# Performance work log

Hardware: AMD Instinct MI355X
Metric: run time of the kernel (lower is better)

Reference implementation:

```python
import jax, jax.numpy as jnp
import numpy as np

B, N, K, D, H = 16384, 10, 5, 512, 2
HD = D // H  # 256
IMG = 512.0


def setup_inputs() -> dict:
    key = jax.random.key(0)
    ks = jax.random.split(key, 18)
    w = lambda k, shape: (jax.random.normal(k, shape) * 0.02).astype(jnp.float32)
    boxes = jax.random.uniform(ks[0], (B, N, 4), minval=0.0, maxval=IMG, dtype=jnp.float32)
    return {
        'boxes': boxes,
        'w_in': w(ks[1], (D, K * 4)), 'b_in': jnp.zeros((D,), jnp.float32),
        'wqkv': w(ks[2], (3 * D, D)), 'bqkv': jnp.zeros((3 * D,), jnp.float32),
        'wo': w(ks[3], (D, D)), 'bo': jnp.zeros((D,), jnp.float32),
        'ln1_w': jnp.ones((D,), jnp.float32), 'ln1_b': jnp.zeros((D,), jnp.float32),
        'w1': w(ks[4], (D, D)), 'b1': jnp.zeros((D,), jnp.float32),
        'w2': w(ks[5], (D, D)), 'b2': jnp.zeros((D,), jnp.float32),
        'ln2_w': jnp.ones((D,), jnp.float32), 'ln2_b': jnp.zeros((D,), jnp.float32),
        'lnf_w': jnp.ones((D,), jnp.float32), 'lnf_b': jnp.zeros((D,), jnp.float32),
    }


def _ln(x, w, b, eps=1e-5):
    mu = jnp.mean(x, -1, keepdims=True)
    var = jnp.mean((x - mu) ** 2, -1, keepdims=True)
    return (x - mu) * jax.lax.rsqrt(var + eps) * w + b


def _relationships(boxes):
    # boxes: [B, N, 4] -> rel: [B, N, K*4]
    cx = (boxes[..., 0] + boxes[..., 2]) * 0.5 / IMG
    cy = (boxes[..., 1] + boxes[..., 3]) * 0.5 / IMG
    bw = jnp.abs(boxes[..., 2] - boxes[..., 0]) / IMG
    bh = jnp.abs(boxes[..., 3] - boxes[..., 1]) / IMG
    feats = jnp.stack([cx, cy, bw, bh], -1)  # [B, N, 4]
    dx = cx[:, :, None] - cx[:, None, :]
    dy = cy[:, :, None] - cy[:, None, :]
    dists = dx * dx + dy * dy  # [B, N, N]
    dists = jnp.where(jnp.eye(N, dtype=bool), jnp.inf, dists)
    _, idx = jax.lax.top_k(-dists, K)  # K smallest, ascending -> [B, N, K]
    nbr = jnp.take_along_axis(jnp.broadcast_to(feats[:, None], (B, N, N, 4)), idx[:, :, :, None], axis=2)  # [B, N, K, 4]
    return (nbr - feats[:, :, None, :]).reshape(B, N, K * 4)


def reference(boxes, w_in, b_in, wqkv, bqkv, wo, bo, ln1_w, ln1_b, w1, b1, w2, b2, ln2_w, ln2_b, lnf_w, lnf_b):
    rel = _relationships(boxes)                      # [B, N, 20]
    x = rel @ w_in.T + b_in                          # [B, N, D]
    # --- self attention (post-norm TransformerEncoderLayer, eval mode: no dropout) ---
    qkv = x @ wqkv.T + bqkv
    q, k, v = jnp.split(qkv, 3, axis=-1)
    split_heads = lambda t: t.reshape(B, N, H, HD).transpose(0, 2, 1, 3)
    q, k, v = split_heads(q), split_heads(k), split_heads(v)
    scores = jnp.einsum('bhqd,bhkd->bhqk', q, k) / jnp.sqrt(jnp.float32(HD))
    att = jax.nn.softmax(scores, axis=-1)
    o = jnp.einsum('bhqk,bhkd->bhqd', att, v).transpose(0, 2, 1, 3).reshape(B, N, D)
    x = _ln(x + o @ wo.T + bo, ln1_w, ln1_b)
    # --- feed forward ---
    ff = jax.nn.gelu(x @ w1.T + b1, approximate=False) @ w2.T + b2
    x = _ln(x + ff, ln2_w, ln2_b)
    return _ln(x, lnf_w, lnf_b)
```

## Files before the change

kernel.cpp:

```cpp
#include <hip/hip_runtime.h>
#include <hip/hip_bf16.h>
#include <math.h>

#define B_   16384
#define NT   10
#define KNN  5
#define D_   512
#define MTOT (B_*NT)

typedef __bf16 bf;
typedef __bf16 bfrag8 __attribute__((ext_vector_type(8)));
typedef float  floatx4 __attribute__((ext_vector_type(4)));

__device__ __forceinline__ float tof(bf x) { return (float)x; }
__device__ __forceinline__ bf    tob(float x) { return (bf)x; }

#define GLD_LDS(g, l) __builtin_amdgcn_global_load_lds( \
    (const __attribute__((address_space(1))) void*)(g), \
    (__attribute__((address_space(3))) void*)(l), 16, 0, 0)

__global__ void prep_folds(const float* __restrict__ wqkv, const float* __restrict__ bqkv,
                           const float* __restrict__ wo,   const float* __restrict__ bo,
                           bf* __restrict__ At, bf* __restrict__ Ct,
                           float* __restrict__ wconst, float* __restrict__ uvec)
{
    int gid = blockIdx.x, tid = threadIdx.x;
    if (gid < 4096) {
        int idx = gid * 256 + tid;
        int mat = idx >> 18;
        int rem = idx & 262143;
        int row = rem >> 9, col = rem & 511;
        float acc = 0.f;
        if (mat < 2) {
            int h = mat;
            const float* wq = wqkv + (size_t)(h * 256) * 512;
            const float* wk = wqkv + (size_t)(512 + h * 256) * 512;
            for (int c = 0; c < 256; ++c)
                acc += wq[c * 512 + col] * wk[c * 512 + row];
            At[(size_t)h * 262144 + row * 512 + col] = tob(acc * 0.0625f);
        } else {
            int h = mat - 2;
            const float* wv = wqkv + (size_t)(1024 + h * 256) * 512;
            for (int e = 0; e < 256; ++e)
                acc += wv[e * 512 + col] * wo[row * 512 + h * 256 + e];
            Ct[(size_t)h * 262144 + row * 512 + col] = tob(acc);
        }
    } else {
        for (int d = tid; d < 512; d += 256) {
            float acc = bo[d];
            for (int e = 0; e < 512; ++e)
                acc += bqkv[1024 + e] * wo[d * 512 + e];
            wconst[d] = acc;
            for (int h = 0; h < 2; ++h) {
                float u = 0.f;
                for (int c = 0; c < 256; ++c)
                    u += wqkv[(size_t)(512 + h * 256 + c) * 512 + d] * bqkv[h * 256 + c];
                uvec[h * 512 + d] = u * 0.0625f;
            }
        }
    }
}

__global__ void cvt_w(const float* __restrict__ src, bf* __restrict__ dst)
{
    int i = blockIdx.x * 256 + threadIdx.x;
    float4 v = *(const float4*)(src + (size_t)i * 4);
    bf4_store: ;
    bf o[4] = { tob(v.x), tob(v.y), tob(v.z), tob(v.w) };
    *(unsigned long long*)(dst + (size_t)i * 4) = *(unsigned long long*)o;
}

__global__ void rel_kernel(const float* __restrict__ boxes, float* __restrict__ rel)
{
#pragma clang fp contract(off)
    int gid = blockIdx.x * blockDim.x + threadIdx.x;
    if (gid >= MTOT) return;
    int b = gid / NT, n = gid % NT;
    const float* bx = boxes + (size_t)b * NT * 4;
    float cx[NT], cy[NT], bw[NT], bh[NT];
#pragma unroll
    for (int j = 0; j < NT; ++j) {
        float x0 = bx[j * 4 + 0], y0 = bx[j * 4 + 1];
        float x1 = bx[j * 4 + 2], y1 = bx[j * 4 + 3];
        cx[j] = ((x0 + x1) * 0.5f) * (1.f / 512.f);
        cy[j] = ((y0 + y1) * 0.5f) * (1.f / 512.f);
        bw[j] = fabsf(x1 - x0) * (1.f / 512.f);
        bh[j] = fabsf(y1 - y0) * (1.f / 512.f);
    }
    float dist[NT];
#pragma unroll
    for (int j = 0; j < NT; ++j) {
        float dx = cx[n] - cx[j], dy = cy[n] - cy[j];
        float dxx = dx * dx, dyy = dy * dy;
        dist[j] = (j == n) ? __builtin_inff() : (dxx + dyy);
    }
    float ocx = cx[n], ocy = cy[n], obw = bw[n], obh = bh[n];
#pragma unroll
    for (int k = 0; k < KNN; ++k) {
        int best = 0; float bd = __builtin_inff();
#pragma unroll
        for (int j = 0; j < NT; ++j)
            if (dist[j] < bd) { bd = dist[j]; best = j; }
        float fx = 0, fy = 0, fw = 0, fh = 0;
#pragma unroll
        for (int j = 0; j < NT; ++j)
            if (j == best) { fx = cx[j]; fy = cy[j]; fw = bw[j]; fh = bh[j]; dist[j] = __builtin_inff(); }
        size_t o = (size_t)gid * 20 + k * 4;
        rel[o + 0] = fx - ocx;
        rel[o + 1] = fy - ocy;
        rel[o + 2] = fw - obw;
        rel[o + 3] = fh - obh;
    }
}

__global__ void gemm_in(const float* __restrict__ rel, const float* __restrict__ w_in,
                        const float* __restrict__ b_in, bf* __restrict__ x0)
{
    __shared__ float relS[128][20];
    int tid = threadIdx.x;
    size_t tok0 = (size_t)blockIdx.x * 128;
    for (int i = tid; i < 128 * 20; i += 256)
        relS[i / 20][i % 20] = rel[tok0 * 20 + i];
    float w0[20], w1r[20];
#pragma unroll
    for (int j = 0; j < 20; ++j) {
        w0[j]  = w_in[tid * 20 + j];
        w1r[j] = w_in[(tid + 256) * 20 + j];
    }
    float bias0 = b_in[tid], bias1 = b_in[tid + 256];
    __syncthreads();
    for (int tk = 0; tk < 128; ++tk) {
        float a0 = bias0, a1 = bias1;
#pragma unroll
        for (int j = 0; j < 20; ++j) {
            float r = relS[tk][j];
            a0 += r * w0[j];
            a1 += r * w1r[j];
        }
        x0[(tok0 + tk) * 512 + tid]       = tob(a0);
        x0[(tok0 + tk) * 512 + tid + 256] = tob(a1);
    }
}

template <int EPI>
__launch_bounds__(256)
__global__ void gemm512(const bf* __restrict__ A, const bf* __restrict__ Bt,
                        bf* __restrict__ out, const float* __restrict__ biasf)
{
    __shared__ bf As[128 * 64];
    __shared__ bf Bs[128 * 64];
    int tid = threadIdx.x;
    int w = tid >> 6, l = tid & 63;
    int lq = l >> 4, lr = l & 15;
    int m0 = blockIdx.y * 128;
    int n0 = blockIdx.x * 128;
    int wm = (w & 1) * 64, wn = (w >> 1) * 64;
    floatx4 acc[4][4] = {};

    for (int kt = 0; kt < 8; ++kt) {
        int kb = kt * 64;
        __syncthreads();
#pragma unroll
        for (int i = 0; i < 4; ++i) {
            int chunk = i * 256 + tid;
            int mm = chunk & 127, kc = chunk >> 7;
            GLD_LDS(A  + (size_t)(m0 + mm) * 512 + kb + kc * 8, As + (i * 256 + w * 64) * 8);
            GLD_LDS(Bt + (size_t)(n0 + mm) * 512 + kb + kc * 8, Bs + (i * 256 + w * 64) * 8);
        }
        __syncthreads();
#pragma unroll
        for (int s = 0; s < 2; ++s) {
            bfrag8 af[4], bfv[4];
#pragma unroll
            for (int i = 0; i < 4; ++i)
                af[i] = *(const bfrag8*)(As + (size_t)((s * 4 + lq) * 128 + wm + i * 16 + lr) * 8);
#pragma unroll
            for (int j = 0; j < 4; ++j)
                bfv[j] = *(const bfrag8*)(Bs + (size_t)((s * 4 + lq) * 128 + wn + j * 16 + lr) * 8);
#pragma unroll
            for (int i = 0; i < 4; ++i)
#pragma unroll
                for (int j = 0; j < 4; ++j)
                    acc[i][j] = __builtin_amdgcn_mfma_f32_16x16x32_bf16(af[i], bfv[j], acc[i][j], 0, 0, 0);
        }
    }
#pragma unroll
    for (int i = 0; i < 4; ++i)
#pragma unroll
        for (int j = 0; j < 4; ++j) {
            int col = n0 + wn + j * 16 + lr;
#pragma unroll
            for (int r = 0; r < 4; ++r) {
                int row = m0 + wm + i * 16 + lq * 4 + r;
                float v = acc[i][j][r];
                if (EPI == 1) { v += biasf[col]; v = 0.5f * v * (1.f + erff(v * 0.70710678118654752f)); }
                if (EPI == 2) v += biasf[col];
                if (EPI == 3) v += tof(out[(size_t)row * 512 + col]);
                out[(size_t)row * 512 + col] = tob(v);
            }
        }
}

__global__ void scores_kernel(const bf* __restrict__ t, const bf* __restrict__ x0,
                              const float* __restrict__ uvec_h, float* __restrict__ att)
{
    int tid = threadIdx.x;
    int w = tid >> 6, l = tid & 63;
    int lq = l >> 4, lr = l & 15;
    size_t b = (size_t)blockIdx.x * 4 + w;
    const bf* trow = t  + (b * NT + lr) * 512;
    const bf* xrow = x0 + (b * NT + lr) * 512;
    floatx4 acc = {0.f, 0.f, 0.f, 0.f};
    float xu = 0.f;
#pragma unroll
    for (int kk = 0; kk < 16; ++kk) {
        bfrag8 a  = *(const bfrag8*)(trow + kk * 32 + lq * 8);
        bfrag8 bb = *(const bfrag8*)(xrow + kk * 32 + lq * 8);
        acc = __builtin_amdgcn_mfma_f32_16x16x32_bf16(a, bb, acc, 0, 0, 0);
#pragma unroll
        for (int jj = 0; jj < 8; ++jj)
            xu += (float)bb[jj] * uvec_h[kk * 32 + lq * 8 + jj];
    }
    xu += __shfl_xor(xu, 16);
    xu += __shfl_xor(xu, 32);
    bool jvalid = (lr < NT);
    float* ab = att + b * 100;
#pragma unroll
    for (int r = 0; r < 4; ++r) {
        float v = jvalid ? (acc[r] + xu) : -__builtin_inff();
        float m = v;
        m = fmaxf(m, __shfl_xor(m, 1)); m = fmaxf(m, __shfl_xor(m, 2));
        m = fmaxf(m, __shfl_xor(m, 4)); m = fmaxf(m, __shfl_xor(m, 8));
        float e = jvalid ? __expf(v - m) : 0.f;
        float s = e;
        s += __shfl_xor(s, 1); s += __shfl_xor(s, 2);
        s += __shfl_xor(s, 4); s += __shfl_xor(s, 8);
        float a = e / s;
        int i = lq * 4 + r;
        if (jvalid && i < NT) ab[i * 10 + lr] = a;
    }
}

__global__ void zmix(const float* __restrict__ att, const bf* __restrict__ x0, bf* __restrict__ z)
{
    __shared__ float xs[NT][512];
    __shared__ float as[100];
    size_t b = blockIdx.x;
    int tid = threadIdx.x;
    const bf* xb = x0 + b * NT * 512;
    for (int i = tid; i < NT * 512; i += 256) xs[i >> 9][i & 511] = tof(xb[i]);
    for (int i = tid; i < 100; i += 256) as[i] = att[b * 100 + i];
    __syncthreads();
    bf* zb = z + b * NT * 512;
    for (int o = tid; o < NT * 512; o += 256) {
        int i = o >> 9, d = o & 511;
        float a = 0.f;
#pragma unroll
        for (int j = 0; j < NT; ++j) a += as[i * 10 + j] * xs[j][d];
        zb[o] = tob(a);
    }
}

__global__ void ln_kernel(const bf* __restrict__ xin, const bf* __restrict__ yin,
                          const float* __restrict__ w, const float* __restrict__ bias,
                          bf* __restrict__ xout)
{
    int tid = threadIdx.x;
    int wv = tid >> 6, l = tid & 63;
    size_t tok = (size_t)blockIdx.x * 4 + wv;
    bfrag8 xv = *(const bfrag8*)(xin + tok * 512 + l * 8);
    bfrag8 yv = *(const bfrag8*)(yin + tok * 512 + l * 8);
    float v[8]; float s = 0.f;
#pragma unroll
    for (int i = 0; i < 8; ++i) { v[i] = (float)xv[i] + (float)yv[i]; s += v[i]; }
#pragma unroll
    for (int m = 1; m < 64; m <<= 1) s += __shfl_xor(s, m);
    float mu = s * (1.f / 512.f);
    float vs = 0.f;
#pragma unroll
    for (int i = 0; i < 8; ++i) { float d = v[i] - mu; vs += d * d; }
#pragma unroll
    for (int m = 1; m < 64; m <<= 1) vs += __shfl_xor(vs, m);
    float r = rsqrtf(vs * (1.f / 512.f) + 1e-5f);
    bfrag8 ov;
#pragma unroll
    for (int i = 0; i < 8; ++i) {
        int d = l * 8 + i;
        ov[i] = tob((v[i] - mu) * r * w[d] + bias[d]);
    }
    *(bfrag8*)(xout + tok * 512 + l * 8) = ov;
}

__global__ void final_kernel(const bf* __restrict__ x1, const bf* __restrict__ ff2,
                             const float* __restrict__ w2, const float* __restrict__ b2,
                             const float* __restrict__ wf, const float* __restrict__ bfi,
                             float* __restrict__ out)
{
    int tid = threadIdx.x;
    int wv = tid >> 6, l = tid & 63;
    size_t tok = (size_t)blockIdx.x * 4 + wv;
    bfrag8 xv = *(const bfrag8*)(x1 + tok * 512 + l * 8);
    bfrag8 yv = *(const bfrag8*)(ff2 + tok * 512 + l * 8);
    float v[8]; float s = 0.f;
#pragma unroll
    for (int i = 0; i < 8; ++i) { v[i] = (float)xv[i] + (float)yv[i]; s += v[i]; }
#pragma unroll
    for (int m = 1; m < 64; m <<= 1) s += __shfl_xor(s, m);
    float mu = s * (1.f / 512.f);
    float vs = 0.f;
#pragma unroll
    for (int i = 0; i < 8; ++i) { float d = v[i] - mu; vs += d * d; }
#pragma unroll
    for (int m = 1; m < 64; m <<= 1) vs += __shfl_xor(vs, m);
    float r = rsqrtf(vs * (1.f / 512.f) + 1e-5f);
    float u[8]; float s2 = 0.f;
#pragma unroll
    for (int i = 0; i < 8; ++i) {
        int d = l * 8 + i;
        u[i] = (v[i] - mu) * r * w2[d] + b2[d];
        s2 += u[i];
    }
#pragma unroll
    for (int m = 1; m < 64; m <<= 1) s2 += __shfl_xor(s2, m);
    float mu2 = s2 * (1.f / 512.f);
    float vs2 = 0.f;
#pragma unroll
    for (int i = 0; i < 8; ++i) { float d = u[i] - mu2; vs2 += d * d; }
#pragma unroll
    for (int m = 1; m < 64; m <<= 1) vs2 += __shfl_xor(vs2, m);
    float r2 = rsqrtf(vs2 * (1.f / 512.f) + 1e-5f);
    float4 o0, o1;
    float* op = (float*)&o0;
#pragma unroll
    for (int i = 0; i < 4; ++i) op[i] = (u[i] - mu2) * r2 * wf[l * 8 + i] + bfi[l * 8 + i];
    op = (float*)&o1;
#pragma unroll
    for (int i = 0; i < 4; ++i) op[i] = (u[4 + i] - mu2) * r2 * wf[l * 8 + 4 + i] + bfi[l * 8 + 4 + i];
    *(float4*)(out + tok * 512 + l * 8) = o0;
    *(float4*)(out + tok * 512 + l * 8 + 4) = o1;
}

extern "C" void kernel_launch(void* const* d_in, const int* in_sizes, int n_in,
                              void* d_out, int out_size, void* d_ws, size_t ws_size,
                              hipStream_t stream)
{
    const float* boxes = (const float*)d_in[0];
    const float* w_in  = (const float*)d_in[1];
    const float* b_in  = (const float*)d_in[2];
    const float* wqkv  = (const float*)d_in[3];
    const float* bqkv  = (const float*)d_in[4];
    const float* wo    = (const float*)d_in[5];
    const float* bo    = (const float*)d_in[6];
    const float* ln1w  = (const float*)d_in[7];
    const float* ln1b  = (const float*)d_in[8];
    const float* w1    = (const float*)d_in[9];
    const float* b1    = (const float*)d_in[10];
    const float* w2    = (const float*)d_in[11];
    const float* b2    = (const float*)d_in[12];
    const float* ln2w  = (const float*)d_in[13];
    const float* ln2b  = (const float*)d_in[14];
    const float* lnfw  = (const float*)d_in[15];
    const float* lnfb  = (const float*)d_in[16];
    float* out = (float*)d_out;

    char* ws = (char*)d_ws;
    bf*    At     = (bf*)(ws + 0);
    bf*    Ct     = (bf*)(ws + 1048576);
    bf*    W1b    = (bf*)(ws + 2097152);
    bf*    W2b    = (bf*)(ws + 2621440);
    float* wconst = (float*)(ws + 3145728);
    float* uvec   = (float*)(ws + 3147776);
    float* att    = (float*)(ws + 3151872);
    bf*    x0     = (bf*)(ws + 16259072);
    bf*    t      = (bf*)(ws + 184047616);
    bf*    y      = (bf*)(ws + 351836160);
    float* rel    = (float*)(ws + 184047616);

    dim3 gblk(256);
    dim3 ggemm(4, MTOT / 128);

    prep_folds<<<4097, gblk, 0, stream>>>(wqkv, bqkv, wo, bo, At, Ct, wconst, uvec);
    cvt_w<<<256, gblk, 0, stream>>>(w1, W1b);
    cvt_w<<<256, gblk, 0, stream>>>(w2, W2b);
    rel_kernel<<<(MTOT + 255) / 256, gblk, 0, stream>>>(boxes, rel);
    gemm_in<<<MTOT / 128, gblk, 0, stream>>>(rel, w_in, b_in, x0);

    gemm512<0><<<ggemm, gblk, 0, stream>>>(x0, At, t, nullptr);
    scores_kernel<<<B_ / 4, gblk, 0, stream>>>(t, x0, uvec, att);
    gemm512<0><<<ggemm, gblk, 0, stream>>>(x0, At + 262144, t, nullptr);
    scores_kernel<<<B_ / 4, gblk, 0, stream>>>(t, x0, uvec + 512, att + (size_t)B_ * 100);
    zmix<<<B_, gblk, 0, stream>>>(att, x0, t);
    gemm512<2><<<ggemm, gblk, 0, stream>>>(t, Ct, y, wconst);
    zmix<<<B_, gblk, 0, stream>>>(att + (size_t)B_ * 100, x0, t);
    gemm512<3><<<ggemm, gblk, 0, stream>>>(t, Ct + 262144, y, nullptr);
    ln_kernel<<<MTOT / 4, gblk, 0, stream>>>(x0, y, ln1w, ln1b, x0);
    gemm512<1><<<ggemm, gblk, 0, stream>>>(x0, W1b, t, b1);
    gemm512<2><<<ggemm, gblk, 0, stream>>>(t, W2b, y, b2);
    final_kernel<<<MTOT / 4, gblk, 0, stream>>>(x0, y, ln2w, ln2b, lnfw, lnfb, out);
}
```

Before: 2.578 ms.

## Rewrite 512-wide GEMM with full-N tiles and double-buffered LDS prefetch

The GEMM kernel now has each 512-thread block compute a full 128x512 output tile, so each A row-block is loaded once rather than four times. The K loop uses 32-wide steps with two LDS buffers, so the next tile's global-to-LDS loads are issued while MFMAs run on the current one, and there is one barrier per step. Each wave holds more accumulators (4x8), which raises register pressure and could limit occupancy despite launch_bounds(512,2).

```diff
diff --git a/kernel.cpp b/kernel.cpp
--- a/kernel.cpp
+++ b/kernel.cpp
@@ -65,7 +65,6 @@
 {
     int i = blockIdx.x * 256 + threadIdx.x;
     float4 v = *(const float4*)(src + (size_t)i * 4);
-    bf4_store: ;
     bf o[4] = { tob(v.x), tob(v.y), tob(v.z), tob(v.w) };
     *(unsigned long long*)(dst + (size_t)i * 4) = *(unsigned long long*)o;
 }
@@ -143,60 +142,74 @@
 }
 
 template <int EPI>
-__launch_bounds__(256)
-__global__ void gemm512(const bf* __restrict__ A, const bf* __restrict__ Bt,
+__launch_bounds__(512, 2)
+__global__ void gemm_fn(const bf* __restrict__ A, const bf* __restrict__ Bt,
                         bf* __restrict__ out, const float* __restrict__ biasf)
 {
-    __shared__ bf As[128 * 64];
-    __shared__ bf Bs[128 * 64];
+    __shared__ bf As[2][128 * 32];
+    __shared__ bf Bs[2][512 * 32];
     int tid = threadIdx.x;
     int w = tid >> 6, l = tid & 63;
     int lq = l >> 4, lr = l & 15;
-    int m0 = blockIdx.y * 128;
-    int n0 = blockIdx.x * 128;
-    int wm = (w & 1) * 64, wn = (w >> 1) * 64;
-    floatx4 acc[4][4] = {};
-
-    for (int kt = 0; kt < 8; ++kt) {
-        int kb = kt * 64;
-        __syncthreads();
-#pragma unroll
-        for (int i = 0; i < 4; ++i) {
-            int chunk = i * 256 + tid;
-            int mm = chunk & 127, kc = chunk >> 7;
-            GLD_LDS(A  + (size_t)(m0 + mm) * 512 + kb + kc * 8, As + (i * 256 + w * 64) * 8);
-            GLD_LDS(Bt + (size_t)(n0 + mm) * 512 + kb + kc * 8, Bs + (i * 256 + w * 64) * 8);
+    size_t m0 = (size_t)blockIdx.x * 128;
+    int wm = (w & 1) * 64, wn = (w >> 1) * 128;
+    floatx4 acc[4][8] = {};
+
+    const bf* Ag = A + (m0 + (tid & 127)) * 512 + (tid >> 7) * 8;
+    const bf* Bg = Bt + (size_t)tid * 512;
+
+    auto stage = [&](int buf, int kt) {
+        GLD_LDS(Ag + kt * 32, &As[buf][w * 512]);
+#pragma unroll
+        for (int p = 0; p < 4; ++p)
+            GLD_LDS(Bg + kt * 32 + p * 8, &Bs[buf][(p * 512 + w * 64) * 8]);
+    };
+
+    stage(0, 0);
+    asm volatile("s_waitcnt vmcnt(0)" ::: "memory");
+    __builtin_amdgcn_s_barrier();
+    __builtin_amdgcn_sched_barrier(0);
+
+#pragma unroll 2
+    for (int kt = 0; kt < 16; ++kt) {
+        int cur = kt & 1;
+        if (kt < 15) stage(cur ^ 1, kt + 1);
+
+        const bf* as = &As[cur][(lq * 128 + wm + lr) * 8];
+        const bf* bs = &Bs[cur][(lq * 512 + wn + lr) * 8];
+        bfrag8 af[4], bfv[8];
+#pragma unroll
+        for (int i = 0; i < 4; ++i)
+            af[i] = *(const bfrag8*)(as + i * 16 * 8);
+#pragma unroll
+        for (int j = 0; j < 8; ++j)
+            bfv[j] = *(const bfrag8*)(bs + j * 16 * 8);
+#pragma unroll
+        for (int i = 0; i < 4; ++i)
+#pragma unroll
+            for (int j = 0; j < 8; ++j)
+                acc[i][j] = __builtin_amdgcn_mfma_f32_16x16x32_bf16(af[i], bfv[j], acc[i][j], 0, 0, 0);
+
+        if (kt < 15) {
+            asm volatile("s_waitcnt vmcnt(0) lgkmcnt(0)" ::: "memory");
+            __builtin_amdgcn_s_barrier();
+            __builtin_amdgcn_sched_barrier(0);
         }
-        __syncthreads();
-#pragma unroll
-        for (int s = 0; s < 2; ++s) {
-            bfrag8 af[4], bfv[4];
-#pragma unroll
-            for (int i = 0; i < 4; ++i)
-                af[i] = *(const bfrag8*)(As + (size_t)((s * 4 + lq) * 128 + wm + i * 16 + lr) * 8);
-#pragma unroll
-            for (int j = 0; j < 4; ++j)
-                bfv[j] = *(const bfrag8*)(Bs + (size_t)((s * 4 + lq) * 128 + wn + j * 16 + lr) * 8);
-#pragma unroll
-            for (int i = 0; i < 4; ++i)
-#pragma unroll
-                for (int j = 0; j < 4; ++j)
-                    acc[i][j] = __builtin_amdgcn_mfma_f32_16x16x32_bf16(af[i], bfv[j], acc[i][j], 0, 0, 0);
-        }
-    }
+    }
+
 #pragma unroll
     for (int i = 0; i < 4; ++i)
 #pragma unroll
-        for (int j = 0; j < 4; ++j) {
-            int col = n0 + wn + j * 16 + lr;
+        for (int j = 0; j < 8; ++j) {
+            int col = wn + j * 16 + lr;
 #pragma unroll
             for (int r = 0; r < 4; ++r) {
-                int row = m0 + wm + i * 16 + lq * 4 + r;
+                int row = wm + i * 16 + lq * 4 + r;
                 float v = acc[i][j][r];
                 if (EPI == 1) { v += biasf[col]; v = 0.5f * v * (1.f + erff(v * 0.70710678118654752f)); }
                 if (EPI == 2) v += biasf[col];
-                if (EPI == 3) v += tof(out[(size_t)row * 512 + col]);
-                out[(size_t)row * 512 + col] = tob(v);
+                if (EPI == 3) v += tof(out[(m0 + row) * 512 + col]);
+                out[(m0 + row) * 512 + col] = tob(v);
             }
         }
 }
@@ -377,7 +390,7 @@
     float* rel    = (float*)(ws + 184047616);
 
     dim3 gblk(256);
-    dim3 ggemm(4, MTOT / 128);
+    dim3 gfn(MTOT / 128);
 
     prep_folds<<<4097, gblk, 0, stream>>>(wqkv, bqkv, wo, bo, At, Ct, wconst, uvec);
     cvt_w<<<256, gblk, 0, stream>>>(w1, W1b);
@@ -385,16 +398,16 @@
     rel_kernel<<<(MTOT + 255) / 256, gblk, 0, stream>>>(boxes, rel);
     gemm_in<<<MTOT / 128, gblk, 0, stream>>>(rel, w_in, b_in, x0);
 
-    gemm512<0><<<ggemm, gblk, 0, stream>>>(x0, At, t, nullptr);
+    gemm_fn<0><<<gfn, 512, 0, stream>>>(x0, At, t, nullptr);
     scores_kernel<<<B_ / 4, gblk, 0, stream>>>(t, x0, uvec, att);
-    gemm512<0><<<ggemm, gblk, 0, stream>>>(x0, At + 262144, t, nullptr);
+    gemm_fn<0><<<gfn, 512, 0, stream>>>(x0, At + 262144, t, nullptr);
     scores_kernel<<<B_ / 4, gblk, 0, stream>>>(t, x0, uvec + 512, att + (size_t)B_ * 100);
     zmix<<<B_, gblk, 0, stream>>>(att, x0, t);
-    gemm512<2><<<ggemm, gblk, 0, stream>>>(t, Ct, y, wconst);
+    gemm_fn<2><<<gfn, 512, 0, stream>>>(t, Ct, y, wconst);
     zmix<<<B_, gblk, 0, stream>>>(att + (size_t)B_ * 100, x0, t);
-    gemm512<3><<<ggemm, gblk, 0, stream>>>(t, Ct + 262144, y, nullptr);
+    gemm_fn<3><<<gfn, 512, 0, stream>>>(t, Ct + 262144, y, nullptr);
     ln_kernel<<<MTOT / 4, gblk, 0, stream>>>(x0, y, ln1w, ln1b, x0);
-    gemm512<1><<<ggemm, gblk, 0, stream>>>(x0, W1b, t, b1);
-    gemm512<2><<<ggemm, gblk, 0, stream>>>(t, W2b, y, b2);
+    gemm_fn<1><<<gfn, 512, 0, stream>>>(x0, W1b, t, b1);
+    gemm_fn<2><<<gfn, 512, 0, stream>>>(t, W2b, y, b2);
     final_kernel<<<MTOT / 4, gblk, 0, stream>>>(x0, y, ln2w, ln2b, lnfw, lnfb, out);
 }
```

New measurement: 2.375 ms. 1.09x faster.
